# Optimization experiments

Hardware: AMD Instinct MI355X
Metric: run time of the kernel (lower is better)

The kernel has to match this reference:

```python
import jax, jax.numpy as jnp
import numpy as np


def _gumbel(key, shape):
    # -log(Exp(1)) == standard Gumbel; matches torch's -empty.exponential_().log()
    u = jax.random.uniform(key, shape, minval=1e-10, maxval=1.0)
    return -jnp.log(-jnp.log(u))


def setup_inputs() -> dict:
    key = jax.random.key(0)
    dims = [(1026, 1024), (3074, 1024), (5122, 512)]
    names = ['wc1', 'wc2', 'wd1', 'wd2', 'gc1', 'gc2', 'gd1', 'gd2']
    inp = {}
    k = key
    for li, (din, dout) in enumerate(dims, start=1):
        for nm in names:
            k, sub = jax.random.split(k)
            if nm.startswith('w'):
                inp[f'l{li}_{nm}'] = jax.random.normal(sub, (din, dout), dtype=jnp.float32)
            else:
                inp[f'l{li}_{nm}'] = _gumbel(sub, (din, dout)).astype(jnp.float32)
    k, kx, kw = jax.random.split(k, 3)
    inp['x'] = jax.random.uniform(kx, (32768, 512), dtype=jnp.float32)
    inp['lin_w'] = jax.random.uniform(kw, (1, 1024), dtype=jnp.float32)
    inp['tau'] = 1
    return inp


def _st_gate(w, g, tau):
    # hard gumbel-softmax over axis 0 with straight-through estimator
    y = jax.nn.softmax((w + g) / tau, axis=0)
    hard = jax.nn.one_hot(jnp.argmax(y, axis=0), w.shape[0], dtype=y.dtype).T
    return hard + y - jax.lax.stop_gradient(y)


def _logic_layer(h, ws, gs, tau, skip):
    wc1, wc2, wd1, wd2 = ws
    gc1, gc2, gd1, gd2 = gs
    c = (h @ _st_gate(wc1, gc1, tau)) * (h @ _st_gate(wc2, gc2, tau))  # AND
    a = h @ _st_gate(wd1, gd1, tau)
    b = h @ _st_gate(wd2, gd2, tau)
    d = 1.0 - (1.0 - a) * (1.0 - b)  # OR
    parts = [h, c, d] if skip else [c, d]
    return jnp.concatenate(parts, axis=-1)


def reference(x, l1_wc1, l1_wc2, l1_wd1, l1_wd2, l1_gc1, l1_gc2, l1_gd1, l1_gd2,
              l2_wc1, l2_wc2, l2_wd1, l2_wd2, l2_gc1, l2_gc2, l2_gd1, l2_gd2,
              l3_wc1, l3_wc2, l3_wd1, l3_wd2, l3_gc1, l3_gc2, l3_gd1, l3_gd2,
              lin_w, tau):
    t = jnp.asarray(tau, dtype=x.dtype)
    B = x.shape[0]
    # InputAugmentor: [x, 1-x, 1, 0]
    h = jnp.concatenate([x, 1.0 - x, jnp.ones((B, 1), x.dtype), jnp.zeros((B, 1), x.dtype)], axis=-1)
    layers = [
        ((l1_wc1, l1_wc2, l1_wd1, l1_wd2), (l1_gc1, l1_gc2, l1_gd1, l1_gd2), True),
        ((l2_wc1, l2_wc2, l2_wd1, l2_wd2), (l2_gc1, l2_gc2, l2_gd1, l2_gd2), True),
        ((l3_wc1, l3_wc2, l3_wd1, l3_wd2), (l3_gc1, l3_gc2, l3_gd1, l3_gd2), False),
    ]
    for ws, gs, skip in layers:
        h = _logic_layer(h, ws, gs, t, skip)
    # nonnegative == False -> weight used as-is
    return (h @ lin_w.T).squeeze(-1)
```

## Files before the change

### kernel.cpp

```cpp
#include <hip/hip_runtime.h>
#include <stdint.h>


struct GatePtrs {
    const float* w[12];
    const float* g[12];
};

__global__ __launch_bounds__(256) void argmax_kernel(GatePtrs gp,
                                                     unsigned long long* __restrict__ packed) {
    const int dins[3]  = {1026, 3074, 5122};
    const int douts[3] = {1024, 1024, 512};
    const int offs[3]  = {0, 4096, 8192};
    int gate  = blockIdx.z;
    int layer = gate >> 2;
    int din  = dins[layer];
    int dout = douts[layer];
    int col = blockIdx.x * 256 + threadIdx.x;
    int r0  = blockIdx.y * 64;
    if (col >= dout || r0 >= din) return;
    int r1 = min(r0 + 64, din);
    const float* __restrict__ w = gp.w[gate];
    const float* __restrict__ g = gp.g[gate];
    float best  = -3.4e38f;
    int bestrow = r0;
    #pragma unroll 4
    for (int i = r0; i < r1; ++i) {
        float v = w[(size_t)i * dout + col] + g[(size_t)i * dout + col];
        if (v > best) { best = v; bestrow = i; }
    }
    unsigned int u   = __float_as_uint(best);
    unsigned int key = u ^ ((u & 0x80000000u) ? 0xFFFFFFFFu : 0x80000000u);
    unsigned long long p = ((unsigned long long)key << 32)
                         | (unsigned long long)(0xFFFFFFFFu - (unsigned int)bestrow);
    atomicMax(packed + offs[layer] + (gate & 3) * dout + col, p);
}

__global__ __launch_bounds__(256) void convert_kernel(const unsigned long long* __restrict__ packed,
                                                      unsigned short* __restrict__ idx) {
    int i = blockIdx.x * 256 + threadIdx.x;
    if (i < 10240) {
        unsigned int low = (unsigned int)(packed[i] & 0xFFFFFFFFull);
        idx[i] = (unsigned short)(0xFFFFFFFFu - low);
    }
}

__global__ __launch_bounds__(256, 7) void forward_kernel(const float* __restrict__ x,
                                                         const float* __restrict__ lin_w,
                                                         const unsigned short* __restrict__ idx,
                                                         float* __restrict__ out) {
    __shared__ float h[5122];
    __shared__ float wsum[4];
    const int row = blockIdx.x;
    const int t   = threadIdx.x;

    const float2* xr = (const float2*)(x + (size_t)row * 512);
    float2 v = xr[t];
    h[2 * t]           = v.x;
    h[2 * t + 1]       = v.y;
    h[512 + 2 * t]     = 1.0f - v.x;
    h[512 + 2 * t + 1] = 1.0f - v.y;
    if (t == 0) { h[1024] = 1.0f; h[1025] = 0.0f; }
    __syncthreads();

    int len  = 1026;
    int ioff = 0;
    #pragma unroll
    for (int layer = 0; layer < 2; ++layer) {
        #pragma unroll
        for (int k = 0; k < 4; ++k) {
            int j  = t + k * 256;
            int i1 = idx[ioff +        j];
            int i2 = idx[ioff + 1024 + j];
            int i3 = idx[ioff + 2048 + j];
            int i4 = idx[ioff + 3072 + j];
            float c = h[i1] * h[i2];
            float a = h[i3], b = h[i4];
            float d = 1.0f - (1.0f - a) * (1.0f - b);
            h[len +        j] = c;
            h[len + 1024 + j] = d;
        }
        __syncthreads();
        len  += 2048;
        ioff += 4096;
    }

    float sum = 0.0f;
    #pragma unroll
    for (int k = 0; k < 2; ++k) {
        int j  = t + k * 256;
        int i1 = idx[8192 +        j];
        int i2 = idx[8192 +  512 + j];
        int i3 = idx[8192 + 1024 + j];
        int i4 = idx[8192 + 1536 + j];
        float c = h[i1] * h[i2];
        float a = h[i3], b = h[i4];
        float d = 1.0f - (1.0f - a) * (1.0f - b);
        sum += lin_w[j] * c + lin_w[512 + j] * d;
    }

    #pragma unroll
    for (int off = 32; off > 0; off >>= 1)
        sum += __shfl_down(sum, off, 64);
    if ((t & 63) == 0) wsum[t >> 6] = sum;
    __syncthreads();
    if (t == 0) out[row] = wsum[0] + wsum[1] + wsum[2] + wsum[3];
}

extern "C" void kernel_launch(void* const* d_in, const int* in_sizes, int n_in,
                              void* d_out, int out_size, void* d_ws, size_t ws_size,
                              hipStream_t stream) {
    GatePtrs gp;
    for (int l = 0; l < 3; ++l) {
        for (int s = 0; s < 4; ++s) {
            gp.w[l * 4 + s] = (const float*)d_in[l * 8 + s];
            gp.g[l * 4 + s] = (const float*)d_in[l * 8 + 4 + s];
        }
    }
    const float* x     = (const float*)d_in[24];
    const float* lin_w = (const float*)d_in[25];
    float* out = (float*)d_out;

    unsigned long long* packed = (unsigned long long*)d_ws;
    unsigned short* idx = (unsigned short*)((char*)d_ws + 10240 * sizeof(unsigned long long));

    hipMemsetAsync(d_ws, 0, 10240 * sizeof(unsigned long long), stream);

    dim3 gridA(4 , 81 , 12 );
    argmax_kernel<<<gridA, 256, 0, stream>>>(gp, packed);

    convert_kernel<<<40, 256, 0, stream>>>(packed, idx);

    forward_kernel<<<32768, 256, 0, stream>>>(x, lin_w, idx, out);
}
```

Measured before the change: 382.3 us.

## Process two batch rows per block with interleaved float2 shared state and pre-scaled index pairs

The forward kernel now handles two batch rows per 512-thread block. Activations are stored interleaved as float2, so each gathered shared-memory load serves both rows, and each gate index is loaded once and reused for two rows. The convert kernel emits byte-offset index pairs as uint2 so the forward kernel loads both operand offsets in one access, and the argmax kernel reads float2 to cover two columns per thread. This halves index traffic and gather instruction count per row, at the cost of 41KB of shared memory per block and larger blocks, which may reduce occupancy.

Measured after the change: 368.8 us. -3.5%, faster.

```diff
diff --git a/kernel.cpp b/kernel.cpp
--- a/kernel.cpp
+++ b/kernel.cpp
@@ -16,95 +16,124 @@
     int layer = gate >> 2;
     int din  = dins[layer];
     int dout = douts[layer];
-    int col = blockIdx.x * 256 + threadIdx.x;
-    int r0  = blockIdx.y * 64;
-    if (col >= dout || r0 >= din) return;
+    int c2 = blockIdx.x * 256 + threadIdx.x;
+    int r0 = blockIdx.y * 64;
+    if (2 * c2 >= dout || r0 >= din) return;
     int r1 = min(r0 + 64, din);
     const float* __restrict__ w = gp.w[gate];
     const float* __restrict__ g = gp.g[gate];
-    float best  = -3.4e38f;
-    int bestrow = r0;
-    #pragma unroll 4
+    float bx = -3.4e38f, by = -3.4e38f;
+    int rx = r0, ry = r0;
+    #pragma unroll 8
     for (int i = r0; i < r1; ++i) {
-        float v = w[(size_t)i * dout + col] + g[(size_t)i * dout + col];
-        if (v > best) { best = v; bestrow = i; }
+        float2 wv = *(const float2*)(w + (size_t)i * dout + 2 * c2);
+        float2 gv = *(const float2*)(g + (size_t)i * dout + 2 * c2);
+        float vx = wv.x + gv.x, vy = wv.y + gv.y;
+        if (vx > bx) { bx = vx; rx = i; }
+        if (vy > by) { by = vy; ry = i; }
     }
-    unsigned int u   = __float_as_uint(best);
-    unsigned int key = u ^ ((u & 0x80000000u) ? 0xFFFFFFFFu : 0x80000000u);
-    unsigned long long p = ((unsigned long long)key << 32)
-                         | (unsigned long long)(0xFFFFFFFFu - (unsigned int)bestrow);
-    atomicMax(packed + offs[layer] + (gate & 3) * dout + col, p);
+    unsigned long long* dst = packed + offs[layer] + (gate & 3) * dout + 2 * c2;
+    unsigned int ux = __float_as_uint(bx);
+    unsigned int kx = ux ^ ((ux & 0x80000000u) ? 0xFFFFFFFFu : 0x80000000u);
+    atomicMax(dst, ((unsigned long long)kx << 32)
+                   | (unsigned long long)(0xFFFFFFFFu - (unsigned int)rx));
+    unsigned int uy = __float_as_uint(by);
+    unsigned int ky = uy ^ ((uy & 0x80000000u) ? 0xFFFFFFFFu : 0x80000000u);
+    atomicMax(dst + 1, ((unsigned long long)ky << 32)
+                   | (unsigned long long)(0xFFFFFFFFu - (unsigned int)ry));
 }
 
 __global__ __launch_bounds__(256) void convert_kernel(const unsigned long long* __restrict__ packed,
-                                                      unsigned short* __restrict__ idx) {
+                                                      uint2* __restrict__ pairs) {
     int i = blockIdx.x * 256 + threadIdx.x;
-    if (i < 10240) {
-        unsigned int low = (unsigned int)(packed[i] & 0xFFFFFFFFull);
-        idx[i] = (unsigned short)(0xFFFFFFFFu - low);
-    }
+    if (i >= 5120) return;
+    int l    = (i < 2048) ? 0 : ((i < 4096) ? 1 : 2);
+    int half = (l == 2) ? 512 : 1024;
+    int r    = i - l * 2048;
+    int type = (r >= half) ? 1 : 0;
+    int g    = r - type * half;
+    int o1   = l * 4096 + 2 * type * half + g;
+    int o2   = o1 + half;
+    unsigned int i1 = 0xFFFFFFFFu - (unsigned int)(packed[o1] & 0xFFFFFFFFull);
+    unsigned int i2 = 0xFFFFFFFFu - (unsigned int)(packed[o2] & 0xFFFFFFFFull);
+    pairs[i] = make_uint2(i1 * 8u, i2 * 8u);
 }
 
-__global__ __launch_bounds__(256, 7) void forward_kernel(const float* __restrict__ x,
-                                                         const float* __restrict__ lin_w,
-                                                         const unsigned short* __restrict__ idx,
-                                                         float* __restrict__ out) {
-    __shared__ float h[5122];
-    __shared__ float wsum[4];
-    const int row = blockIdx.x;
-    const int t   = threadIdx.x;
+__global__ __launch_bounds__(512) void forward_kernel(const float* __restrict__ x,
+                                                      const float* __restrict__ lin_w,
+                                                      const uint2* __restrict__ pairs,
+                                                      float* __restrict__ out) {
+    __shared__ float2 hp[5122];
+    __shared__ float2 red[8];
+    const int t  = threadIdx.x;
+    const int r0 = blockIdx.x * 2;
+    const char* hb = (const char*)hp;
 
-    const float2* xr = (const float2*)(x + (size_t)row * 512);
-    float2 v = xr[t];
-    h[2 * t]           = v.x;
-    h[2 * t + 1]       = v.y;
-    h[512 + 2 * t]     = 1.0f - v.x;
-    h[512 + 2 * t + 1] = 1.0f - v.y;
-    if (t == 0) { h[1024] = 1.0f; h[1025] = 0.0f; }
+    float xa = x[(size_t)r0 * 512 + t];
+    float xb = x[(size_t)(r0 + 1) * 512 + t];
+    uint2 pa0 = pairs[t], pa1 = pairs[512 + t];
+    uint2 po0 = pairs[1024 + t], po1 = pairs[1536 + t];
+    hp[t]       = make_float2(xa, xb);
+    hp[512 + t] = make_float2(1.0f - xa, 1.0f - xb);
+    if (t == 0) { hp[1024] = make_float2(1.0f, 1.0f); hp[1025] = make_float2(0.0f, 0.0f); }
     __syncthreads();
 
-    int len  = 1026;
-    int ioff = 0;
-    #pragma unroll
-    for (int layer = 0; layer < 2; ++layer) {
-        #pragma unroll
-        for (int k = 0; k < 4; ++k) {
-            int j  = t + k * 256;
-            int i1 = idx[ioff +        j];
-            int i2 = idx[ioff + 1024 + j];
-            int i3 = idx[ioff + 2048 + j];
-            int i4 = idx[ioff + 3072 + j];
-            float c = h[i1] * h[i2];
-            float a = h[i3], b = h[i4];
-            float d = 1.0f - (1.0f - a) * (1.0f - b);
-            h[len +        j] = c;
-            h[len + 1024 + j] = d;
-        }
-        __syncthreads();
-        len  += 2048;
-        ioff += 4096;
+    {
+        float2 a0 = *(const float2*)(hb + pa0.x), b0 = *(const float2*)(hb + pa0.y);
+        float2 a1 = *(const float2*)(hb + pa1.x), b1 = *(const float2*)(hb + pa1.y);
+        float2 e0 = *(const float2*)(hb + po0.x), f0 = *(const float2*)(hb + po0.y);
+        float2 e1 = *(const float2*)(hb + po1.x), f1 = *(const float2*)(hb + po1.y);
+        hp[1026 + t]       = make_float2(a0.x * b0.x, a0.y * b0.y);
+        hp[1538 + t]       = make_float2(a1.x * b1.x, a1.y * b1.y);
+        hp[2050 + t]       = make_float2(1.0f - (1.0f - e0.x) * (1.0f - f0.x),
+                                         1.0f - (1.0f - e0.y) * (1.0f - f0.y));
+        hp[2562 + t]       = make_float2(1.0f - (1.0f - e1.x) * (1.0f - f1.x),
+                                         1.0f - (1.0f - e1.y) * (1.0f - f1.y));
     }
+    uint2 qa0 = pairs[2048 + t], qa1 = pairs[2560 + t];
+    uint2 qo0 = pairs[3072 + t], qo1 = pairs[3584 + t];
+    __syncthreads();
 
-    float sum = 0.0f;
-    #pragma unroll
-    for (int k = 0; k < 2; ++k) {
-        int j  = t + k * 256;
-        int i1 = idx[8192 +        j];
-        int i2 = idx[8192 +  512 + j];
-        int i3 = idx[8192 + 1024 + j];
-        int i4 = idx[8192 + 1536 + j];
-        float c = h[i1] * h[i2];
-        float a = h[i3], b = h[i4];
-        float d = 1.0f - (1.0f - a) * (1.0f - b);
-        sum += lin_w[j] * c + lin_w[512 + j] * d;
+    {
+        float2 a0 = *(const float2*)(hb + qa0.x), b0 = *(const float2*)(hb + qa0.y);
+        float2 a1 = *(const float2*)(hb + qa1.x), b1 = *(const float2*)(hb + qa1.y);
+        float2 e0 = *(const float2*)(hb + qo0.x), f0 = *(const float2*)(hb + qo0.y);
+        float2 e1 = *(const float2*)(hb + qo1.x), f1 = *(const float2*)(hb + qo1.y);
+        hp[3074 + t]       = make_float2(a0.x * b0.x, a0.y * b0.y);
+        hp[3586 + t]       = make_float2(a1.x * b1.x, a1.y * b1.y);
+        hp[4098 + t]       = make_float2(1.0f - (1.0f - e0.x) * (1.0f - f0.x),
+                                         1.0f - (1.0f - e0.y) * (1.0f - f0.y));
+        hp[4610 + t]       = make_float2(1.0f - (1.0f - e1.x) * (1.0f - f1.x),
+                                         1.0f - (1.0f - e1.y) * (1.0f - f1.y));
+    }
+    uint2 za = pairs[4096 + t], zo = pairs[4608 + t];
+    float wA = lin_w[t], wO = lin_w[512 + t];
+    __syncthreads();
+
+    float2 s;
+    {
+        float2 a = *(const float2*)(hb + za.x), b = *(const float2*)(hb + za.y);
+        float2 e = *(const float2*)(hb + zo.x), f = *(const float2*)(hb + zo.y);
+        float cx = a.x * b.x, cy = a.y * b.y;
+        float dx = 1.0f - (1.0f - e.x) * (1.0f - f.x);
+        float dy = 1.0f - (1.0f - e.y) * (1.0f - f.y);
+        s.x = wA * cx + wO * dx;
+        s.y = wA * cy + wO * dy;
     }
 
     #pragma unroll
-    for (int off = 32; off > 0; off >>= 1)
-        sum += __shfl_down(sum, off, 64);
-    if ((t & 63) == 0) wsum[t >> 6] = sum;
+    for (int off = 32; off > 0; off >>= 1) {
+        s.x += __shfl_down(s.x, off, 64);
+        s.y += __shfl_down(s.y, off, 64);
+    }
+    if ((t & 63) == 0) red[t >> 6] = s;
     __syncthreads();
-    if (t == 0) out[row] = wsum[0] + wsum[1] + wsum[2] + wsum[3];
+    if (t == 0) {
+        float2 tot = red[0];
+        #pragma unroll
+        for (int i = 1; i < 8; ++i) { tot.x += red[i].x; tot.y += red[i].y; }
+        *(float2*)(out + r0) = tot;
+    }
 }
 
 extern "C" void kernel_launch(void* const* d_in, const int* in_sizes, int n_in,
@@ -122,14 +151,14 @@
     float* out = (float*)d_out;
 
     unsigned long long* packed = (unsigned long long*)d_ws;
-    unsigned short* idx = (unsigned short*)((char*)d_ws + 10240 * sizeof(unsigned long long));
+    uint2* pairs = (uint2*)((char*)d_ws + 10240 * sizeof(unsigned long long));
 
     hipMemsetAsync(d_ws, 0, 10240 * sizeof(unsigned long long), stream);
 
-    dim3 gridA(4 , 81 , 12 );
+    dim3 gridA(2 , 81 , 12 );
     argmax_kernel<<<gridA, 256, 0, stream>>>(gp, packed);
 
-    convert_kernel<<<40, 256, 0, stream>>>(packed, idx);
+    convert_kernel<<<20, 256, 0, stream>>>(packed, pairs);
 
-    forward_kernel<<<32768, 256, 0, stream>>>(x, lin_w, idx, out);
+    forward_kernel<<<16384, 512, 0, stream>>>(x, lin_w, pairs, out);
 }
```
